# Kernel tuning notes

Measured on AMD Instinct MI355X. Metric: run time of the kernel, lower is better.

The kernel has to match this reference:

```python
import jax, jax.numpy as jnp
import numpy as np

B, CIN, COUT, K, H, W = 8, 512, 512, 3, 64, 64
SCALE = 1.0 / np.sqrt(CIN * K * K).astype(np.float32)  # conv.scale
LRELU_SCALE = 1.4142135623730951  # sqrt(2), FusedLeakyReLU scale


def setup_inputs() -> dict:
    key = jax.random.key(0)
    ks = jax.random.split(key, 6)
    return {
        "x": jax.random.normal(ks[0], (B, CIN, H, W), jnp.float32),
        "style": jax.random.normal(ks[1], (B, CIN), jnp.float32),
        "noise": jax.random.normal(ks[2], (1, 1, H, W), jnp.float32),
        "weight": jax.random.normal(ks[3], (COUT, CIN, K, K), jnp.float32),
        "bias": jnp.zeros((COUT,), jnp.float32),
        "noise_strength": jax.random.uniform(ks[4], (1,), jnp.float32),
    }


def reference(x, style, noise, weight, bias, noise_strength):
    # Modulate: scale * weight * style  -> [B, Cout, Cin, K, K]
    w = SCALE * weight[None] * style[:, None, :, None, None]
    # Demodulate per (batch, out_channel)
    demod = jax.lax.rsqrt(jnp.sum(w * w, axis=(2, 3, 4)) + 1e-8)
    w = w * demod[:, :, None, None, None]
    # Per-sample conv (grouped-conv trick in torch) via vmap over batch
    pad = K // 2
    def conv_one(xi, wi):  # xi: [Cin,H,W], wi: [Cout,Cin,K,K]
        return jax.lax.conv_general_dilated(
            xi[None], wi, window_strides=(1, 1),
            padding=[(pad, pad), (pad, pad)],
            dimension_numbers=("NCHW", "OIHW", "NCHW"))[0]
    out = jax.vmap(conv_one)(x, w)  # [B, Cout, H, W]
    # NoiseInjection: out + strength * noise (noise broadcast over B, C)
    out = out + noise_strength[0] * noise
    # FusedLeakyReLU: leaky_relu(out + bias, 0.2) * sqrt(2)
    y = out + bias[None, :, None, None]
    return jnp.where(y >= 0, y, 0.2 * y) * LRELU_SCALE
```

## Files before the change

kernel.cpp:

```cpp
#include <hip/hip_runtime.h>
#include <hip/hip_bf16.h>

typedef __attribute__((ext_vector_type(8))) short s16x8;
typedef __attribute__((ext_vector_type(4))) float f32x4;

#define MOD_SCALE 0.014731391274719739f
#define CIPAD 40

__global__ __launch_bounds__(256) void k_border(__hip_bfloat16* __restrict__ xs) {
    const int idx = blockIdx.x * 256 + threadIdx.x;
    const int b = idx / 16640;
    const int r2 = idx - b * 16640;
    const int pair = r2 >> 6;
    const int ciq = r2 & 63;
    int pr, pc;
    if (pair < 66)       { pr = 0;          pc = pair; }
    else if (pair < 132) { pr = 65;         pc = pair - 66; }
    else if (pair < 196) { pr = pair - 131; pc = 0; }
    else                 { pr = pair - 195; pc = 65; }
    uint4* d = (uint4*)(xs + (((size_t)b * 66 + pr) * 66 + pc) * 512) + ciq;
    *d = make_uint4(0u, 0u, 0u, 0u);
}

__global__ __launch_bounds__(256) void k_xprep(const float* __restrict__ x,
                                               const float* __restrict__ style,
                                               __hip_bfloat16* __restrict__ xs) {
    const int cig = blockIdx.x, h = blockIdx.y, b = blockIdx.z;
    const int ci0 = cig * 128;
    __shared__ __align__(16) __hip_bfloat16 tile[64][130];
    const int t = threadIdx.x;
    const int wl = t & 63, cl4 = t >> 6;
    for (int r = 0; r < 32; ++r) {
        int c = r * 4 + cl4;
        float v = x[(((size_t)b * 512 + ci0 + c) * 64 + h) * 64 + wl];
        float s = style[b * 512 + ci0 + c];
        tile[wl][c] = __float2bfloat16(v * s * MOD_SCALE);
    }
    __syncthreads();
    const int w4 = t >> 6;
    const int cp = (t & 63) * 2;
    for (int r = 0; r < 16; ++r) {
        int w = r * 4 + w4;
        unsigned v = *(const unsigned*)(&tile[w][cp]);
        *(unsigned*)(&xs[(((size_t)b * 66 + h + 1) * 66 + (w + 1)) * 512 +
                         ci0 + cp]) = v;
    }
}

__global__ __launch_bounds__(256) void k_wprep(const float* __restrict__ w,
                                               __hip_bfloat16* __restrict__ wb) {
    const int idx = blockIdx.x * 256 + threadIdx.x;
    const float* src = w + (size_t)idx * 9;
#pragma unroll
    for (int tap = 0; tap < 9; ++tap)
        wb[(size_t)tap * 262144 + idx] = __float2bfloat16(src[tap]);
}

__global__ __launch_bounds__(256) void k_demod(const float* __restrict__ w,
                                               const float* __restrict__ style,
                                               float* __restrict__ dem) {
    const int co = blockIdx.x;
    const int t = threadIdx.x;
    float accb[8] = {0.f, 0.f, 0.f, 0.f, 0.f, 0.f, 0.f, 0.f};
    for (int ci = t; ci < 512; ci += 256) {
        const float* wp = w + ((size_t)co * 512 + ci) * 9;
        float ws = 0.f;
#pragma unroll
        for (int k = 0; k < 9; ++k) { float v = wp[k]; ws += v * v; }
#pragma unroll
        for (int bb = 0; bb < 8; ++bb) {
            float s = style[bb * 512 + ci];
            accb[bb] += s * s * ws;
        }
    }
    __shared__ float red[256];
    const float S2 = MOD_SCALE * MOD_SCALE;
    for (int bb = 0; bb < 8; ++bb) {
        red[t] = accb[bb];
        __syncthreads();
        for (int off = 128; off > 0; off >>= 1) {
            if (t < off) red[t] += red[t + off];
            __syncthreads();
        }
        if (t == 0) dem[bb * 512 + co] = rsqrtf(S2 * red[0] + 1e-8f);
        __syncthreads();
    }
}

__global__ __launch_bounds__(256, 2) void k_conv(
    const __hip_bfloat16* __restrict__ xs,
    const __hip_bfloat16* __restrict__ wb,
    const float* __restrict__ demod,
    const float* __restrict__ noise,
    const float* __restrict__ bias,
    const float* __restrict__ nstr,
    float* __restrict__ out) {
    __shared__ __align__(16) __hip_bfloat16 Xl[4 * 66 * CIPAD];
    __shared__ __align__(16) __hip_bfloat16 Wl[3 * 128 * CIPAD];

    const int t = threadIdx.x;
    const int bi = blockIdx.x;
    const int co0 = (bi & 3) * 128;
    const int h0 = ((bi >> 2) & 31) * 2;
    const int b = bi >> 7;
    const int lane = t & 63;
    const int wv = t >> 6;
    const int wm = wv & 1, wn = wv >> 1;
    const int q = lane >> 4, ln = lane & 15;

    f32x4 acc[4][4];
#pragma unroll
    for (int i = 0; i < 4; ++i)
#pragma unroll
        for (int j = 0; j < 4; ++j) acc[i][j] = (f32x4){0.f, 0.f, 0.f, 0.f};

    const int xp_r = t / 66, xp_c = t - xp_r * 66;
    const int wco = t >> 1, wpart = t & 1;

    const __hip_bfloat16* xsb = xs + (size_t)b * 66 * 66 * 512;

    for (int cb = 0; cb < 16; ++cb) {
        const int ci0 = cb * 32;
        __syncthreads();
        {
            const float4* s =
                (const float4*)(xsb + (((h0 + xp_r) * 66 + xp_c) << 9) + ci0);
            float4 v0 = s[0], v1 = s[1], v2 = s[2], v3 = s[3];
            float4* d = (float4*)(Xl + (xp_r * 66 + xp_c) * CIPAD);
            d[0] = v0; d[1] = v1; d[2] = v2; d[3] = v3;
            if (t < 8) {
                const float4* s2 =
                    (const float4*)(xsb + (((h0 + 3) * 66 + 58 + t) << 9) + ci0);
                float4 u0 = s2[0], u1 = s2[1], u2 = s2[2], u3 = s2[3];
                float4* d2 = (float4*)(Xl + (3 * 66 + 58 + t) * CIPAD);
                d2[0] = u0; d2[1] = u1; d2[2] = u2; d2[3] = u3;
            }
        }
#pragma unroll
        for (int rr = 0; rr < 3; ++rr) {
            const float4* s = (const float4*)(wb + (size_t)rr * 262144 +
                                              ((co0 + wco) << 9) + ci0 + wpart * 16);
            float4 v0 = s[0], v1 = s[1];
            float4* d = (float4*)(Wl + (rr * 128 + wco) * CIPAD + wpart * 16);
            d[0] = v0; d[1] = v1;
        }
        __syncthreads();

        for (int dh = 0; dh < 3; ++dh) {
            if (dh) {
                __syncthreads();
#pragma unroll
                for (int rr = 0; rr < 3; ++rr) {
                    const float4* s =
                        (const float4*)(wb + (size_t)(dh * 3 + rr) * 262144 +
                                        ((co0 + wco) << 9) + ci0 + wpart * 16);
                    float4 v0 = s[0], v1 = s[1];
                    float4* d =
                        (float4*)(Wl + (rr * 128 + wco) * CIPAD + wpart * 16);
                    d[0] = v0; d[1] = v1;
                }
                __syncthreads();
            }
            const int xrow = dh + wn;
#pragma unroll
            for (int dw = 0; dw < 3; ++dw) {
                s16x8 af[4], bfr[4];
#pragma unroll
                for (int mi = 0; mi < 4; ++mi)
                    af[mi] = *(const s16x8*)(Wl +
                        (dw * 128 + wm * 64 + mi * 16 + ln) * CIPAD + q * 8);
#pragma unroll
                for (int ni = 0; ni < 4; ++ni)
                    bfr[ni] = *(const s16x8*)(Xl +
                        (xrow * 66 + ni * 16 + ln + dw) * CIPAD + q * 8);
#pragma unroll
                for (int mi = 0; mi < 4; ++mi)
#pragma unroll
                    for (int ni = 0; ni < 4; ++ni)
                        acc[mi][ni] = __builtin_amdgcn_mfma_f32_16x16x32_bf16(
                            af[mi], bfr[ni], acc[mi][ni], 0, 0, 0);
            }
        }
    }

    const float nsv = nstr[0];
    const int h = h0 + wn;
    const float LR = 1.4142135623730951f;
#pragma unroll
    for (int mi = 0; mi < 4; ++mi) {
        float dm[4], bs[4];
#pragma unroll
        for (int r = 0; r < 4; ++r) {
            int co = co0 + wm * 64 + mi * 16 + q * 4 + r;
            dm[r] = demod[b * 512 + co];
            bs[r] = bias[co];
        }
#pragma unroll
        for (int ni = 0; ni < 4; ++ni) {
            int w = ni * 16 + ln;
            float nz = nsv * noise[h * 64 + w];
#pragma unroll
            for (int r = 0; r < 4; ++r) {
                int co = co0 + wm * 64 + mi * 16 + q * 4 + r;
                float v = acc[mi][ni][r] * dm[r] + nz + bs[r];
                v = (v >= 0.f ? v : 0.2f * v) * LR;
                out[(((size_t)b * 512 + co) * 64 + h) * 64 + w] = v;
            }
        }
    }
}

extern "C" void kernel_launch(void* const* d_in, const int* in_sizes, int n_in,
                              void* d_out, int out_size, void* d_ws, size_t ws_size,
                              hipStream_t stream) {
    const float* x      = (const float*)d_in[0];
    const float* style  = (const float*)d_in[1];
    const float* noise  = (const float*)d_in[2];
    const float* weight = (const float*)d_in[3];
    const float* bias   = (const float*)d_in[4];
    const float* nstr   = (const float*)d_in[5];
    float* out = (float*)d_out;

    char* ws = (char*)d_ws;
    __hip_bfloat16* xs = (__hip_bfloat16*)ws;
    __hip_bfloat16* wb = (__hip_bfloat16*)(ws + 35684352);
    float* demod = (float*)(ws + 35684352 + 4718592);

    k_border<<<520, 256, 0, stream>>>(xs);
    k_xprep<<<dim3(4, 64, 8), 256, 0, stream>>>(x, style, xs);
    k_wprep<<<1024, 256, 0, stream>>>(weight, wb);
    k_demod<<<512, 256, 0, stream>>>(weight, style, demod);
    k_conv<<<1024, 256, 0, stream>>>(xs, wb, demod, noise, bias, nstr, out);
}
```

Measured before the change: 310.3 us.

## Use direct global-to-LDS loads with XOR-swizzled layout in conv kernel

Replaces the register-staged global→LDS copies in the conv kernel with global_load_lds 16-byte direct transfers. The padded CIPAD layout becomes an unpadded 64-byte-row layout with an XOR swizzle to avoid bank conflicts, with per-thread source pointers precomputed. The aim is to cut VGPR pressure and load instructions, so occupancy is raised to 3 blocks per CU via launch_bounds. The weight-prep kernel also stages through LDS to coalesce its reads. The LDS transfers are still synchronous behind barriers, so there is no double buffering, and raising the occupancy target may force register spills.

```diff
diff --git a/kernel.cpp b/kernel.cpp
--- a/kernel.cpp
+++ b/kernel.cpp
@@ -5,7 +5,12 @@
 typedef __attribute__((ext_vector_type(4))) float f32x4;
 
 #define MOD_SCALE 0.014731391274719739f
-#define CIPAD 40
+
+__device__ __forceinline__ void gload_lds16(const void* g, void* l) {
+    __builtin_amdgcn_global_load_lds(
+        (const __attribute__((address_space(1))) unsigned int*)g,
+        (__attribute__((address_space(3))) unsigned int*)l, 16, 0, 0);
+}
 
 __global__ __launch_bounds__(256) void k_border(__hip_bfloat16* __restrict__ xs) {
     const int idx = blockIdx.x * 256 + threadIdx.x;
@@ -49,11 +54,16 @@
 
 __global__ __launch_bounds__(256) void k_wprep(const float* __restrict__ w,
                                                __hip_bfloat16* __restrict__ wb) {
-    const int idx = blockIdx.x * 256 + threadIdx.x;
-    const float* src = w + (size_t)idx * 9;
+    __shared__ float lds[2304];
+    const int t = threadIdx.x;
+    const int p0 = blockIdx.x * 256;
+    const float* src = w + (size_t)p0 * 9;
+#pragma unroll
+    for (int k = 0; k < 9; ++k) lds[k * 256 + t] = src[k * 256 + t];
+    __syncthreads();
 #pragma unroll
     for (int tap = 0; tap < 9; ++tap)
-        wb[(size_t)tap * 262144 + idx] = __float2bfloat16(src[tap]);
+        wb[(size_t)tap * 262144 + p0 + t] = __float2bfloat16(lds[t * 9 + tap]);
 }
 
 __global__ __launch_bounds__(256) void k_demod(const float* __restrict__ w,
@@ -87,7 +97,7 @@
     }
 }
 
-__global__ __launch_bounds__(256, 2) void k_conv(
+__global__ __launch_bounds__(256, 3) void k_conv(
     const __hip_bfloat16* __restrict__ xs,
     const __hip_bfloat16* __restrict__ wb,
     const float* __restrict__ demod,
@@ -95,8 +105,8 @@
     const float* __restrict__ bias,
     const float* __restrict__ nstr,
     float* __restrict__ out) {
-    __shared__ __align__(16) __hip_bfloat16 Xl[4 * 66 * CIPAD];
-    __shared__ __align__(16) __hip_bfloat16 Wl[3 * 128 * CIPAD];
+    __shared__ __align__(16) char Xl[264 * 64];
+    __shared__ __align__(16) char Wl[384 * 64];
 
     const int t = threadIdx.x;
     const int bi = blockIdx.x;
@@ -114,65 +124,70 @@
 #pragma unroll
         for (int j = 0; j < 4; ++j) acc[i][j] = (f32x4){0.f, 0.f, 0.f, 0.f};
 
-    const int xp_r = t / 66, xp_c = t - xp_r * 66;
-    const int wco = t >> 1, wpart = t & 1;
-
-    const __hip_bfloat16* xsb = xs + (size_t)b * 66 * 66 * 512;
+    const char* xsb = (const char*)xs + (size_t)b * 66 * 66 * 1024;
+    const char* xsrc[4];
+#pragma unroll
+    for (int i = 0; i < 4; ++i) {
+        int g = i * 256 + t;
+        int e = g >> 2, s = g & 3;
+        int r = e / 66, c = e - r * 66;
+        int gc = s ^ (e & 3);
+        xsrc[i] = xsb + (size_t)((h0 + r) * 66 + c) * 1024 + gc * 16;
+    }
+    const char* xsrct = xsb;
+    {
+        int e = 256 + (t >> 2), s = t & 3;
+        int c = e - 198;
+        int gc = s ^ (e & 3);
+        xsrct = xsb + (size_t)((h0 + 3) * 66 + c) * 1024 + gc * 16;
+    }
+    const char* wsrc[6];
+#pragma unroll
+    for (int i = 0; i < 6; ++i) {
+        int g = i * 256 + t;
+        int e = g >> 2, s = g & 3;
+        int rr = e >> 7, co = e & 127;
+        int gc = s ^ (co & 3);
+        wsrc[i] = (const char*)wb +
+                  ((size_t)rr * 262144 + (size_t)(co0 + co) * 512) * 2 + gc * 16;
+    }
+    char* ldsXw = Xl + (wv << 10);
+    char* ldsWw = Wl + (wv << 10);
 
     for (int cb = 0; cb < 16; ++cb) {
-        const int ci0 = cb * 32;
-        __syncthreads();
-        {
-            const float4* s =
-                (const float4*)(xsb + (((h0 + xp_r) * 66 + xp_c) << 9) + ci0);
-            float4 v0 = s[0], v1 = s[1], v2 = s[2], v3 = s[3];
-            float4* d = (float4*)(Xl + (xp_r * 66 + xp_c) * CIPAD);
-            d[0] = v0; d[1] = v1; d[2] = v2; d[3] = v3;
-            if (t < 8) {
-                const float4* s2 =
-                    (const float4*)(xsb + (((h0 + 3) * 66 + 58 + t) << 9) + ci0);
-                float4 u0 = s2[0], u1 = s2[1], u2 = s2[2], u3 = s2[3];
-                float4* d2 = (float4*)(Xl + (3 * 66 + 58 + t) * CIPAD);
-                d2[0] = u0; d2[1] = u1; d2[2] = u2; d2[3] = u3;
-            }
-        }
-#pragma unroll
-        for (int rr = 0; rr < 3; ++rr) {
-            const float4* s = (const float4*)(wb + (size_t)rr * 262144 +
-                                              ((co0 + wco) << 9) + ci0 + wpart * 16);
-            float4 v0 = s[0], v1 = s[1];
-            float4* d = (float4*)(Wl + (rr * 128 + wco) * CIPAD + wpart * 16);
-            d[0] = v0; d[1] = v1;
-        }
+        const int cboff = cb * 64;
+        __syncthreads();
+#pragma unroll
+        for (int i = 0; i < 4; ++i)
+            gload_lds16(xsrc[i] + cboff, ldsXw + i * 4096);
+        if (t < 32) gload_lds16(xsrct + cboff, Xl + 16384);
+#pragma unroll
+        for (int i = 0; i < 6; ++i)
+            gload_lds16(wsrc[i] + cboff, ldsWw + i * 4096);
         __syncthreads();
 
         for (int dh = 0; dh < 3; ++dh) {
             if (dh) {
                 __syncthreads();
 #pragma unroll
-                for (int rr = 0; rr < 3; ++rr) {
-                    const float4* s =
-                        (const float4*)(wb + (size_t)(dh * 3 + rr) * 262144 +
-                                        ((co0 + wco) << 9) + ci0 + wpart * 16);
-                    float4 v0 = s[0], v1 = s[1];
-                    float4* d =
-                        (float4*)(Wl + (rr * 128 + wco) * CIPAD + wpart * 16);
-                    d[0] = v0; d[1] = v1;
-                }
+                for (int i = 0; i < 6; ++i)
+                    gload_lds16(wsrc[i] + dh * 1572864 + cboff, ldsWw + i * 4096);
                 __syncthreads();
             }
             const int xrow = dh + wn;
 #pragma unroll
             for (int dw = 0; dw < 3; ++dw) {
                 s16x8 af[4], bfr[4];
+                const char* abase =
+                    Wl + (dw * 128 + wm * 64 + ln) * 64 + ((q ^ (ln & 3)) << 4);
 #pragma unroll
                 for (int mi = 0; mi < 4; ++mi)
-                    af[mi] = *(const s16x8*)(Wl +
-                        (dw * 128 + wm * 64 + mi * 16 + ln) * CIPAD + q * 8);
+                    af[mi] = *(const s16x8*)(abase + mi * 1024);
+                const int ecol = xrow * 66 + dw + ln;
+                const char* bbase = Xl + ecol * 64 + ((q ^ (ecol & 3)) << 4);
 #pragma unroll
                 for (int ni = 0; ni < 4; ++ni)
-                    bfr[ni] = *(const s16x8*)(Xl +
-                        (xrow * 66 + ni * 16 + ln + dw) * CIPAD + q * 8);
+                    bfr[ni] = *(const s16x8*)(bbase + ni * 1024);
 #pragma unroll
                 for (int mi = 0; mi < 4; ++mi)
 #pragma unroll
```

Result: faster. 289.0 us (-6.9%).
